# Kernel tuning notes

Measured on AMD Instinct MI355X. Metric: run time of the kernel, lower is better.

Reference implementation:

```python
import jax, jax.numpy as jnp
import numpy as np
from jax import lax


def setup_inputs() -> dict:
    key = jax.random.key(0)
    ks = jax.random.split(key, 8)
    B, T, F, H = 256, 96, 32, 1024
    s = 0.05
    return {
        "initial_input": jax.random.normal(ks[0], (B, 1, F), jnp.float32),
        "hidden_h": jax.random.normal(ks[1], (B, H), jnp.float32),
        "hidden_c": jax.random.normal(ks[2], (B, H), jnp.float32),
        "targets": jax.random.normal(ks[3], (B, T, F), jnp.float32),
        "W_x": jax.random.normal(ks[4], (F, 4 * H), jnp.float32) * s,
        "W_h": jax.random.normal(ks[5], (H, 4 * H), jnp.float32) * s,
        "b": jnp.zeros((4 * H,), jnp.float32),
        "W_dense": jax.random.normal(ks[6], (H, F), jnp.float32) * s,
        "b_dense": jnp.zeros((F,), jnp.float32),
    }


def reference(initial_input, hidden_h, hidden_c, targets, W_x, W_h, b, W_dense, b_dense):
    # Inference-mode (training=False) decode: no teacher forcing, each step's
    # dense output is fed back as the next LSTM input. Keras LSTM gate order: i, f, c(g), o.
    T = targets.shape[1]

    def step(carry, _):
        h, c, x = carry  # h,c: [B,H], x: [B,F]
        z = x @ W_x + h @ W_h + b            # [B, 4H]
        i, f, g, o = jnp.split(z, 4, axis=-1)
        i = jax.nn.sigmoid(i)
        f = jax.nn.sigmoid(f)
        g = jnp.tanh(g)
        o = jax.nn.sigmoid(o)
        c_new = f * c + i * g
        h_new = o * jnp.tanh(c_new)
        y = h_new @ W_dense + b_dense        # [B, F]
        return (h_new, c_new, y), y

    x0 = initial_input[:, 0, :]              # [B, F]
    _, ys = lax.scan(step, (hidden_h, hidden_c, x0), None, length=T)
    return jnp.transpose(ys, (1, 0, 2))      # [B, T, F]
```

## Files before the change

### kernel.cpp

```cpp
#include <hip/hip_runtime.h>
#include <hip/hip_bf16.h>
#include <stdint.h>

#define B_SZ 256
#define H_SZ 1024
#define NG   4096
#define F_SZ 32
#define T_SZ 96

typedef __attribute__((ext_vector_type(8))) short short8;
typedef __attribute__((ext_vector_type(4))) float f32x4;

__device__ __forceinline__ unsigned short f2bf(float x) {
  unsigned int u = __float_as_uint(x);
  u += 0x7fffu + ((u >> 16) & 1u);
  return (unsigned short)(u >> 16);
}
__device__ __forceinline__ float sigf(float x) {
  return 1.f / (1.f + __expf(-x));
}
__device__ __forceinline__ float tanh_fast(float x) {
  float e = __expf(-2.f * fabsf(x));
  float t = (1.f - e) / (1.f + e);
  return copysignf(t, x);
}
__device__ __forceinline__ void stage16(const void* g, void* l) {
  __builtin_amdgcn_global_load_lds(
      (const __attribute__((address_space(1))) void*)g,
      (__attribute__((address_space(3))) void*)l, 16, 0, 0);
}
__device__ __forceinline__ short8 u4s8(uint4 v) {
  union { uint4 u; short8 s; } c; c.u = v; return c.s;
}

__global__ __launch_bounds__(256) void k_prep_w(
    const float* __restrict__ Wx, const float* __restrict__ Wh,
    const float* __restrict__ Wd,
    unsigned short* __restrict__ WeffT, unsigned short* __restrict__ WhT,
    unsigned short* __restrict__ WdT, unsigned int* __restrict__ flags)
{
  int tid = threadIdx.x;
  if (blockIdx.x == 512) {
    for (int i = 0; i < 17; ++i) flags[i * 256 + tid] = 0u;
    for (int i = 0; i < 128; ++i) {
      int idx = i * 256 + tid;
      int f = idx >> 10, k = idx & 1023;
      WdT[idx] = f2bf(Wd[k * 32 + f]);
    }
    return;
  }
  __shared__ float wx[32 * 256];
  __shared__ unsigned short resE[32 * 256];
  __shared__ unsigned short resH[32 * 256];
  int kt = blockIdx.x & 31, nt = blockIdx.x >> 5;
  int k0 = kt * 32, n0 = nt * 256;
  for (int i = 0; i < 32; ++i) {
    int lin = i * 256 + tid;
    wx[lin] = Wx[(size_t)(lin >> 8) * NG + n0 + (lin & 255)];
  }
  __syncthreads();
  for (int kr = 0; kr < 32; ++kr) {
    int k = k0 + kr;
    float v = Wh[(size_t)k * NG + n0 + tid];
    float acc = 0.f;
#pragma unroll
    for (int f = 0; f < 32; ++f) acc += Wd[k * 32 + f] * wx[f * 256 + tid];
    resH[kr * 256 + tid] = f2bf(v);
    resE[kr * 256 + tid] = f2bf(v + acc);
  }
  __syncthreads();
#pragma unroll
  for (int pass = 0; pass < 2; ++pass) {
    const unsigned short* res = pass ? resH : resE;
    unsigned short* dst = (pass ? WhT : WeffT) + (size_t)(n0 + tid) * H_SZ + k0;
    unsigned int vals[16];
#pragma unroll
    for (int p = 0; p < 16; ++p)
      vals[p] = (unsigned int)res[(2 * p) * 256 + tid] |
                ((unsigned int)res[(2 * p + 1) * 256 + tid] << 16);
#pragma unroll
    for (int qd = 0; qd < 4; ++qd) {
      uint4 v4; v4.x = vals[4*qd]; v4.y = vals[4*qd+1]; v4.z = vals[4*qd+2]; v4.w = vals[4*qd+3];
      ((uint4*)dst)[qd] = v4;
    }
  }
}

__global__ __launch_bounds__(512, 2) void k_persist(
    const unsigned short* __restrict__ WeffT,
    const unsigned short* __restrict__ WhT,
    const float* __restrict__ x0,
    const float* __restrict__ h0,
    const float* __restrict__ c0,
    const float* __restrict__ Wx,
    const float* __restrict__ bvec,
    const float* __restrict__ bd,
    const unsigned short* __restrict__ WdT,
    unsigned short* __restrict__ hbuf0,
    unsigned short* __restrict__ hbuf1,
    float* __restrict__ out,
    unsigned int* __restrict__ flags)
{
  const int b = blockIdx.x;
  const int xcd = b & 7, slot = b >> 3;
  const int m0 = xcd << 5;
  const int nh = slot << 5;
  const int tid = threadIdx.x, lane = tid & 63, w = tid >> 6;
  const int g = w >> 1;
  const int nhh = (w & 1) << 4;

  __shared__ unsigned short Ab[32 * 1024];
  __shared__ float zlds[4][32][33];
  __shared__ float yp[16][32];
  __shared__ unsigned int sPure;

  unsigned int* xcctab = flags + 4096;
  unsigned int myxcc;
  asm volatile("s_getreg_b32 %0, hwreg(HW_REG_XCC_ID)" : "=s"(myxcc));
  myxcc &= 15u;

  float creg[2];
#pragma unroll
  for (int e = 0; e < 2; ++e) {
    int idx = e * 512 + tid;
    int m = idx >> 5, cc = idx & 31;
    size_t gi = (size_t)(m0 + m) * H_SZ + nh + cc;
    hbuf0[gi] = f2bf(h0[gi]);
    creg[e] = c0[gi];
  }
  __syncthreads();
  unsigned int* myflag = flags + (((xcd << 5) | slot) << 4);
  if (tid == 0) {
    __hip_atomic_store(&xcctab[b], myxcc, __ATOMIC_RELAXED,
                       __HIP_MEMORY_SCOPE_AGENT);
    __hip_atomic_store(myflag, 1u, __ATOMIC_RELEASE,
                       __HIP_MEMORY_SCOPE_AGENT);
  }

  const int col = lane & 15;
  const int kq = lane >> 4;
  const int n0a = (g << 10) + nh + nhh + col;
  float bfv = bvec[n0a];
  float u0r[2][4];
#pragma unroll
  for (int mf = 0; mf < 2; ++mf)
#pragma unroll
    for (int e = 0; e < 4; ++e) u0r[mf][e] = bfv;
  for (int f = 0; f < 32; ++f) {
    float wxf = Wx[(size_t)f * NG + n0a];
    bfv += bd[f] * wxf;
#pragma unroll
    for (int mf = 0; mf < 2; ++mf)
#pragma unroll
      for (int e = 0; e < 4; ++e) {
        float xv = x0[(m0 + mf * 16 + (kq << 2) + e) * 32 + f];
        u0r[mf][e] += xv * wxf;
      }
  }

  uint4 wr[32];
  {
    const unsigned short* p0 = WhT + (size_t)n0a * H_SZ + (kq << 3);
#pragma unroll
    for (int kk = 0; kk < 32; ++kk) wr[kk] = *(const uint4*)(p0 + kk * 32);
#pragma unroll
    for (int kk = 0; kk < 32; ++kk)
      asm volatile("" : "+v"(wr[kk].x), "+v"(wr[kk].y),
                        "+v"(wr[kk].z), "+v"(wr[kk].w));
  }

  const int srow = (tid & 127) >> 2;
  const int skg  = (tid & 3) ^ ((tid >> 3) & 3);
  const int sgbase = srow * H_SZ + ((tid >> 7) << 5) + (skg << 3);
  const int wdst = w << 9;
  const int q = kq ^ ((col >> 1) & 3);
  const int aoff = col * 32 + (q << 3);
  const int yf = tid & 31, ykc = tid >> 5;
  const int ysw = (slot >> 1) & 3;
  const unsigned short* wdp = WdT + (size_t)yf * H_SZ + ykc * 64;

  bool pure = false;
  for (int j = 0; j <= T_SZ; ++j) {
    {
      const unsigned int tgt = (unsigned)(j + 1);
      if (w == 0 && lane < 32) {
        const unsigned int* fp = flags + (((xcd << 5) | lane) << 4);
        while (__hip_atomic_load(fp, __ATOMIC_RELAXED, __HIP_MEMORY_SCOPE_AGENT) < tgt)
          __builtin_amdgcn_s_sleep(1);
      }
      __syncthreads();
    }
    if (j == 0) {
      __builtin_amdgcn_fence(__ATOMIC_ACQUIRE, "agent");
      bool eq = true;
      if (w == 0 && lane < 32)
        eq = (__hip_atomic_load(&xcctab[(lane << 3) | xcd], __ATOMIC_RELAXED,
                                __HIP_MEMORY_SCOPE_AGENT) == myxcc);
      unsigned long long bal = __ballot(eq);
      if (tid == 0) sPure = (bal == ~0ull) ? 1u : 0u;
      __syncthreads();
      pure = (sPure != 0u);
    } else if (pure) {
      asm volatile("buffer_inv sc0" ::: "memory");
    } else {
      __builtin_amdgcn_fence(__ATOMIC_ACQUIRE, "agent");
    }
    const unsigned short* hp = (j & 1) ? hbuf1 : hbuf0;
    unsigned short* hn = (j & 1) ? hbuf0 : hbuf1;

    {
      const unsigned short* src = hp + (size_t)m0 * H_SZ + sgbase;
#pragma unroll
      for (int it = 0; it < 8; ++it)
        stage16(src + it * 128, &Ab[it * 4096 + wdst]);
      __syncthreads();
    }

    if (j >= 1) {
      float acc = 0.f;
#pragma unroll
      for (int c2 = 0; c2 < 2; ++c2)
#pragma unroll
        for (int p = 0; p < 4; ++p) {
          uint4 av = *(const uint4*)(Ab + (ykc * 2 + c2) * 1024 + slot * 32 + p * 8);
          uint4 wv = *(const uint4*)(wdp + c2 * 32 + ((p ^ ysw) << 3));
          acc += __uint_as_float(av.x << 16) * __uint_as_float(wv.x << 16);
          acc += __uint_as_float(av.x & 0xffff0000u) * __uint_as_float(wv.x & 0xffff0000u);
          acc += __uint_as_float(av.y << 16) * __uint_as_float(wv.y << 16);
          acc += __uint_as_float(av.y & 0xffff0000u) * __uint_as_float(wv.y & 0xffff0000u);
          acc += __uint_as_float(av.z << 16) * __uint_as_float(wv.z << 16);
          acc += __uint_as_float(av.z & 0xffff0000u) * __uint_as_float(wv.z & 0xffff0000u);
          acc += __uint_as_float(av.w << 16) * __uint_as_float(wv.w << 16);
          acc += __uint_as_float(av.w & 0xffff0000u) * __uint_as_float(wv.w & 0xffff0000u);
        }
      yp[ykc][yf] = acc;
    }

    if (j < T_SZ) {
      f32x4 acc2[2];
#pragma unroll
      for (int mf = 0; mf < 2; ++mf)
#pragma unroll
        for (int e = 0; e < 4; ++e)
          acc2[mf][e] = (j == 0) ? u0r[mf][e] : bfv;
#pragma unroll
      for (int kk = 0; kk < 32; ++kk) {
        short8 bfr = u4s8(wr[kk]);
        short8 a0 = *(const short8*)(Ab + kk * 1024 + aoff);
        short8 a1 = *(const short8*)(Ab + kk * 1024 + 512 + aoff);
        acc2[0] = __builtin_amdgcn_mfma_f32_16x16x32_bf16(a0, bfr, acc2[0], 0, 0, 0);
        acc2[1] = __builtin_amdgcn_mfma_f32_16x16x32_bf16(a1, bfr, acc2[1], 0, 0, 0);
      }
      if (j == 0) {
        const unsigned short* p0 = WeffT + (size_t)n0a * H_SZ + (kq << 3);
#pragma unroll
        for (int kk = 0; kk < 32; ++kk) wr[kk] = *(const uint4*)(p0 + kk * 32);
#pragma unroll
        for (int kk = 0; kk < 32; ++kk)
          asm volatile("" : "+v"(wr[kk].x), "+v"(wr[kk].y),
                            "+v"(wr[kk].z), "+v"(wr[kk].w));
      }
#pragma unroll
      for (int mf = 0; mf < 2; ++mf)
#pragma unroll
        for (int e = 0; e < 4; ++e)
          zlds[g][mf * 16 + (kq << 2) + e][nhh + col] = acc2[mf][e];
    }
    __syncthreads();

    if (j < T_SZ) {
#pragma unroll
      for (int e = 0; e < 2; ++e) {
        int idx = e * 512 + tid;
        int m = idx >> 5, cc = idx & 31;
        float zi = zlds[0][m][cc];
        float zf = zlds[1][m][cc];
        float zg = zlds[2][m][cc];
        float zo = zlds[3][m][cc];
        float iv = sigf(zi), fv = sigf(zf), gv = tanh_fast(zg), ov = sigf(zo);
        float cn = fv * creg[e] + iv * gv;
        creg[e] = cn;
        hn[(size_t)(m0 + m) * H_SZ + nh + cc] = f2bf(ov * tanh_fast(cn));
      }
    }
    if (j >= 1 && tid < 32) {
      float s = bd[tid];
#pragma unroll
      for (int kc = 0; kc < 16; ++kc) s += yp[kc][tid];
      out[(size_t)(m0 + slot) * (T_SZ * F_SZ) + (size_t)(j - 1) * F_SZ + tid] = s;
    }
    __syncthreads();
    if (tid == 0 && j < T_SZ) {
      if (pure)
        __hip_atomic_store(myflag, (unsigned)(j + 2), __ATOMIC_RELAXED,
                           __HIP_MEMORY_SCOPE_AGENT);
      else
        __hip_atomic_store(myflag, (unsigned)(j + 2), __ATOMIC_RELEASE,
                           __HIP_MEMORY_SCOPE_AGENT);
    }
  }
}

extern "C" void kernel_launch(void* const* d_in, const int* in_sizes, int n_in,
                              void* d_out, int out_size, void* d_ws, size_t ws_size,
                              hipStream_t stream)
{
  const float* x0 = (const float*)d_in[0];
  const float* h0 = (const float*)d_in[1];
  const float* c0 = (const float*)d_in[2];
  const float* Wx = (const float*)d_in[4];
  const float* Wh = (const float*)d_in[5];
  const float* bv = (const float*)d_in[6];
  const float* Wd = (const float*)d_in[7];
  const float* bd = (const float*)d_in[8];
  float* out = (float*)d_out;

  char* p = (char*)d_ws;
  unsigned short* WeffT = (unsigned short*)p; p += (size_t)NG * H_SZ * 2;
  unsigned short* WhT   = (unsigned short*)p; p += (size_t)NG * H_SZ * 2;
  unsigned short* WdT   = (unsigned short*)p; p += (size_t)F_SZ * H_SZ * 2;
  unsigned short* hb0   = (unsigned short*)p; p += (size_t)B_SZ * H_SZ * 2;
  unsigned short* hb1   = (unsigned short*)p; p += (size_t)B_SZ * H_SZ * 2;
  unsigned int* flags   = (unsigned int*)p;  p += 4352 * 4;
  (void)ws_size; (void)in_sizes; (void)n_in; (void)out_size;

  k_prep_w<<<dim3(513), dim3(256), 0, stream>>>(Wx, Wh, Wd, WeffT, WhT, WdT, flags);

  k_persist<<<dim3(256), dim3(512), 0, stream>>>(
      WeffT, WhT, x0, h0, c0, Wx, bv, bd, WdT, hb0, hb1, out, flags);
}
```

Before: 811.4 us.

## Poll flags from all waves, bypass L2 on staging, split MFMA chains

Each wave now polls the 32 peer flags itself with __all instead of wave 0 polling and a block barrier. The buffer_inv in the pure-XCC path is dropped, and the h-state staging loads use a cache-coherence bit (sc0) instead. The MFMA K-loop is split into two independent accumulator chains to shorten the dependency chain. The sigmoid/tanh divides become hardware reciprocals, and the dense-output write moves after the flag release so peers are signalled earlier. The goal is lower per-timestep synchronization latency, at the cost of more polling traffic and possible cache-coherence risks.

```diff
diff --git a/kernel.cpp b/kernel.cpp
--- a/kernel.cpp
+++ b/kernel.cpp
@@ -17,17 +17,18 @@
   return (unsigned short)(u >> 16);
 }
 __device__ __forceinline__ float sigf(float x) {
-  return 1.f / (1.f + __expf(-x));
+  float e = __expf(-x);
+  return __builtin_amdgcn_rcpf(1.f + e);
 }
 __device__ __forceinline__ float tanh_fast(float x) {
   float e = __expf(-2.f * fabsf(x));
-  float t = (1.f - e) / (1.f + e);
+  float t = (1.f - e) * __builtin_amdgcn_rcpf(1.f + e);
   return copysignf(t, x);
 }
-__device__ __forceinline__ void stage16(const void* g, void* l) {
+__device__ __forceinline__ void stage16c(const void* g, void* l) {
   __builtin_amdgcn_global_load_lds(
       (const __attribute__((address_space(1))) void*)g,
-      (__attribute__((address_space(3))) void*)l, 16, 0, 0);
+      (__attribute__((address_space(3))) void*)l, 16, 0, 1 );
 }
 __device__ __forceinline__ short8 u4s8(uint4 v) {
   union { uint4 u; short8 s; } c; c.u = v; return c.s;
@@ -112,7 +113,6 @@
   __shared__ unsigned short Ab[32 * 1024];
   __shared__ float zlds[4][32][33];
   __shared__ float yp[16][32];
-  __shared__ unsigned int sPure;
 
   unsigned int* xcctab = flags + 4096;
   unsigned int myxcc;
@@ -178,31 +178,26 @@
   const int yf = tid & 31, ykc = tid >> 5;
   const int ysw = (slot >> 1) & 3;
   const unsigned short* wdp = WdT + (size_t)yf * H_SZ + ykc * 64;
+  const unsigned int* pollp = flags + (((xcd << 5) | (lane & 31)) << 4);
 
   bool pure = false;
   for (int j = 0; j <= T_SZ; ++j) {
     {
       const unsigned int tgt = (unsigned)(j + 1);
-      if (w == 0 && lane < 32) {
-        const unsigned int* fp = flags + (((xcd << 5) | lane) << 4);
-        while (__hip_atomic_load(fp, __ATOMIC_RELAXED, __HIP_MEMORY_SCOPE_AGENT) < tgt)
-          __builtin_amdgcn_s_sleep(1);
-      }
-      __syncthreads();
+      while (true) {
+        unsigned int v = __hip_atomic_load(pollp, __ATOMIC_RELAXED,
+                                           __HIP_MEMORY_SCOPE_AGENT);
+        if (__all(v >= tgt)) break;
+        __builtin_amdgcn_s_sleep(1);
+      }
     }
     if (j == 0) {
       __builtin_amdgcn_fence(__ATOMIC_ACQUIRE, "agent");
-      bool eq = true;
-      if (w == 0 && lane < 32)
-        eq = (__hip_atomic_load(&xcctab[(lane << 3) | xcd], __ATOMIC_RELAXED,
-                                __HIP_MEMORY_SCOPE_AGENT) == myxcc);
-      unsigned long long bal = __ballot(eq);
-      if (tid == 0) sPure = (bal == ~0ull) ? 1u : 0u;
-      __syncthreads();
-      pure = (sPure != 0u);
-    } else if (pure) {
-      asm volatile("buffer_inv sc0" ::: "memory");
-    } else {
+      bool eq = (__hip_atomic_load(&xcctab[((lane & 31) << 3) | xcd],
+                                   __ATOMIC_RELAXED,
+                                   __HIP_MEMORY_SCOPE_AGENT) == myxcc);
+      pure = __all(eq);
+    } else if (!pure) {
       __builtin_amdgcn_fence(__ATOMIC_ACQUIRE, "agent");
     }
     const unsigned short* hp = (j & 1) ? hbuf1 : hbuf0;
@@ -212,7 +207,7 @@
       const unsigned short* src = hp + (size_t)m0 * H_SZ + sgbase;
 #pragma unroll
       for (int it = 0; it < 8; ++it)
-        stage16(src + it * 128, &Ab[it * 4096 + wdst]);
+        stage16c(src + it * 128, &Ab[it * 4096 + wdst]);
       __syncthreads();
     }
 
@@ -237,19 +232,26 @@
     }
 
     if (j < T_SZ) {
-      f32x4 acc2[2];
+      f32x4 accE[2], accO[2];
 #pragma unroll
       for (int mf = 0; mf < 2; ++mf)
 #pragma unroll
-        for (int e = 0; e < 4; ++e)
-          acc2[mf][e] = (j == 0) ? u0r[mf][e] : bfv;
-#pragma unroll
-      for (int kk = 0; kk < 32; ++kk) {
-        short8 bfr = u4s8(wr[kk]);
-        short8 a0 = *(const short8*)(Ab + kk * 1024 + aoff);
-        short8 a1 = *(const short8*)(Ab + kk * 1024 + 512 + aoff);
-        acc2[0] = __builtin_amdgcn_mfma_f32_16x16x32_bf16(a0, bfr, acc2[0], 0, 0, 0);
-        acc2[1] = __builtin_amdgcn_mfma_f32_16x16x32_bf16(a1, bfr, acc2[1], 0, 0, 0);
+        for (int e = 0; e < 4; ++e) {
+          accE[mf][e] = (j == 0) ? u0r[mf][e] : bfv;
+          accO[mf][e] = 0.f;
+        }
+#pragma unroll
+      for (int kk = 0; kk < 32; kk += 2) {
+        short8 b0 = u4s8(wr[kk]);
+        short8 b1 = u4s8(wr[kk + 1]);
+        short8 a00 = *(const short8*)(Ab + kk * 1024 + aoff);
+        short8 a01 = *(const short8*)(Ab + kk * 1024 + 512 + aoff);
+        short8 a10 = *(const short8*)(Ab + (kk + 1) * 1024 + aoff);
+        short8 a11 = *(const short8*)(Ab + (kk + 1) * 1024 + 512 + aoff);
+        accE[0] = __builtin_amdgcn_mfma_f32_16x16x32_bf16(a00, b0, accE[0], 0, 0, 0);
+        accE[1] = __builtin_amdgcn_mfma_f32_16x16x32_bf16(a01, b0, accE[1], 0, 0, 0);
+        accO[0] = __builtin_amdgcn_mfma_f32_16x16x32_bf16(a10, b1, accO[0], 0, 0, 0);
+        accO[1] = __builtin_amdgcn_mfma_f32_16x16x32_bf16(a11, b1, accO[1], 0, 0, 0);
       }
       if (j == 0) {
         const unsigned short* p0 = WeffT + (size_t)n0a * H_SZ + (kq << 3);
@@ -264,7 +266,7 @@
       for (int mf = 0; mf < 2; ++mf)
 #pragma unroll
         for (int e = 0; e < 4; ++e)
-          zlds[g][mf * 16 + (kq << 2) + e][nhh + col] = acc2[mf][e];
+          zlds[g][mf * 16 + (kq << 2) + e][nhh + col] = accE[mf][e] + accO[mf][e];
     }
     __syncthreads();
 
@@ -283,12 +285,6 @@
         hn[(size_t)(m0 + m) * H_SZ + nh + cc] = f2bf(ov * tanh_fast(cn));
       }
     }
-    if (j >= 1 && tid < 32) {
-      float s = bd[tid];
-#pragma unroll
-      for (int kc = 0; kc < 16; ++kc) s += yp[kc][tid];
-      out[(size_t)(m0 + slot) * (T_SZ * F_SZ) + (size_t)(j - 1) * F_SZ + tid] = s;
-    }
     __syncthreads();
     if (tid == 0 && j < T_SZ) {
       if (pure)
@@ -297,6 +293,12 @@
       else
         __hip_atomic_store(myflag, (unsigned)(j + 2), __ATOMIC_RELEASE,
                            __HIP_MEMORY_SCOPE_AGENT);
+    }
+    if (j >= 1 && tid < 32) {
+      float s = bd[tid];
+#pragma unroll
+      for (int kc = 0; kc < 16; ++kc) s += yp[kc][tid];
+      out[(size_t)(m0 + slot) * (T_SZ * F_SZ) + (size_t)(j - 1) * F_SZ + tid] = s;
     }
   }
 }
```

Result: faster. 794.7 us (-2.1%).
